# Kernel tuning notes

Hardware: AMD Instinct MI355X
Metric: run time of the kernel (lower is better)

The kernel has to match this reference:

```python
import jax, jax.numpy as jnp
import numpy as np

N = 200_000          # nodes
E = 6_400_000        # directed edges (before self loops)
F_IN, F_OUT = 20, 10
NEG_SLOPE = 0.2      # PyG GATConv default
BN_EPS = 1e-5


def setup_inputs() -> dict:
    key = jax.random.key(0)
    ks = jax.random.split(key, 20)
    s = 0.1
    return {
        "h": jax.random.normal(ks[0], (N, F_IN), jnp.float32),
        "edge_index": jax.random.randint(ks[1], (2, E), 0, N, dtype=jnp.int64),
        "edge_weight": jax.random.uniform(ks[2], (E, 1), dtype=jnp.float32),
        # BatchNorm1d(20) affine params
        "bn_w": jnp.ones((F_IN,), jnp.float32),
        "bn_b": jnp.zeros((F_IN,), jnp.float32),
        # GATConv params (heads=1): lin (no bias), att vectors, edge lin, output bias
        "W": jax.random.normal(ks[3], (F_OUT, F_IN), jnp.float32) * s,
        "att_src": jax.random.normal(ks[4], (F_OUT,), jnp.float32) * s,
        "att_dst": jax.random.normal(ks[5], (F_OUT,), jnp.float32) * s,
        "att_edge": jax.random.normal(ks[6], (F_OUT,), jnp.float32) * s,
        "W_edge": jax.random.normal(ks[7], (F_OUT, 1), jnp.float32) * s,
        "bias": jax.random.normal(ks[8], (F_OUT,), jnp.float32) * s,
        # dense MLP
        "fc1_w": jax.random.normal(ks[9], (F_OUT, F_OUT), jnp.float32) * s,
        "fc1_b": jnp.zeros((F_OUT,), jnp.float32),
        "fc2_w": jax.random.normal(ks[10], (F_OUT, F_OUT), jnp.float32) * s,
        "fc2_b": jnp.zeros((F_OUT,), jnp.float32),
        "fc3_w": jax.random.normal(ks[11], (F_OUT, F_OUT), jnp.float32) * s,
        "fc3_b": jnp.zeros((F_OUT,), jnp.float32),
    }


def reference(h, edge_index, edge_weight, bn_w, bn_b, W, att_src, att_dst,
              att_edge, W_edge, bias, fc1_w, fc1_b, fc2_w, fc2_b, fc3_w, fc3_b):
    # --- BatchNorm1d (training mode: batch stats, biased variance) ---
    mu = h.mean(axis=0)
    var = jnp.var(h, axis=0)
    xn = (h - mu) * jax.lax.rsqrt(var + BN_EPS) * bn_w + bn_b   # [N, 20]

    # --- GATConv (heads=1, edge_dim=1, add_self_loops, fill_value='mean') ---
    xp = xn @ W.T                       # [N, 10] projected node features
    a_s = xp @ att_src                  # [N] per-node source attention term
    a_d = xp @ att_dst                  # [N] per-node dest attention term

    loop = jnp.arange(N, dtype=edge_index.dtype)
    src = jnp.concatenate([edge_index[0], loop])          # [E+N]
    dst = jnp.concatenate([edge_index[1], loop])          # [E+N]
    loop_attr = jnp.broadcast_to(edge_weight.mean(axis=0), (N, 1))
    ea = jnp.concatenate([edge_weight, loop_attr], axis=0)  # [E+N, 1]

    a_e = (ea @ W_edge.T) @ att_edge                       # [E+N]
    logits = jax.nn.leaky_relu(a_s[src] + a_d[dst] + a_e, NEG_SLOPE)

    # segment softmax over destination neighborhoods (every node has a self loop)
    m = jax.ops.segment_max(logits, dst, num_segments=N)
    ex = jnp.exp(logits - m[dst])
    denom = jax.ops.segment_sum(ex, dst, num_segments=N)
    alpha = ex / denom[dst]                                # [E+N]

    msg = xp[src] * alpha[:, None]                         # [E+N, 10]
    out = jax.ops.segment_sum(msg, dst, num_segments=N) + bias  # [N, 10]

    embeddings = jax.nn.relu(out)
    y = jax.nn.relu(out @ fc1_w.T + fc1_b)
    y = jax.nn.relu(y @ fc2_w.T + fc2_b)
    y = y @ fc3_w.T + fc3_b
    return embeddings, y
```

## Files before the change

### kernel.cpp

```cpp
#include <hip/hip_runtime.h>
#include <hip/hip_fp16.h>

#define NN 200000
#define NE 6400000
#define F_IN 20
#define F_OUT 10
#define NEG_SLOPE 0.2f
#define BN_EPS 1e-5f

#define NPB 256
#define NBUCK 782
#define CHUNK 8192
#define NBLK 782
#define SB 512
#define SSB 1024
#define SNPT (CHUNK / SSB)
#define SZ (NBUCK * NBLK)
#define SCANB 1024
#define G1 ((SZ + SCANB - 1) / SCANB)
#define PREB 120
#define RT 1024
#define MAXB 9216
#define CNPT ((MAXB + RT - 1) / RT)

#define OFF_C      41
#define OFF_LOOPAE 42
#define OFF_PART   128
#define OFF_PEW    (OFF_PART + PREB * 40)
#define OFF_AD     (OFF_PEW + NBLK)
#define OFF_XPA    (((OFF_AD + NN) + 3) & ~3)
#define OFF_XPB    (OFF_XPA + 4 * NN)
#define OFF_SCN    (OFF_XPB + 2 * NN)
#define OFF_BS     (OFF_SCN + SZ + 1)
#define OFF_M      (((OFF_BS + 1024) + 1) & ~1)
#define OFF_REC    OFF_M

typedef unsigned long long u64;

__global__ void __launch_bounds__(SB) k_pre(
        const float* __restrict__ h, const int* __restrict__ ei,
        float* __restrict__ part, int* __restrict__ M) {
    int t = threadIdx.x;
    if (blockIdx.x < PREB) {
        float s[F_IN], q[F_IN];
#pragma unroll
        for (int f = 0; f < F_IN; ++f) { s[f] = 0.f; q[f] = 0.f; }
        for (int i = blockIdx.x * SB + t; i < NN; i += PREB * SB) {
            const float4* row = (const float4*)(h + (size_t)i * F_IN);
#pragma unroll
            for (int v = 0; v < 5; ++v) {
                float4 x = row[v];
                int f = v * 4;
                s[f+0] += x.x; q[f+0] += x.x * x.x;
                s[f+1] += x.y; q[f+1] += x.y * x.y;
                s[f+2] += x.z; q[f+2] += x.z * x.z;
                s[f+3] += x.w; q[f+3] += x.w * x.w;
            }
        }
#pragma unroll
        for (int f = 0; f < F_IN; ++f)
            for (int o = 32; o > 0; o >>= 1) {
                s[f] += __shfl_down(s[f], o);
                q[f] += __shfl_down(q[f], o);
            }
        __shared__ float red[8][40];
        int wave = t >> 6, lane = t & 63;
        if (lane == 0) {
#pragma unroll
            for (int f = 0; f < F_IN; ++f) { red[wave][f] = s[f]; red[wave][F_IN + f] = q[f]; }
        }
        __syncthreads();
        if (t < 40) {
            float a = 0.f;
#pragma unroll
            for (int w8 = 0; w8 < 8; ++w8) a += red[w8][t];
            part[blockIdx.x * 40 + t] = a;
        }
    } else {
        __shared__ int hist[NBUCK];
        int blk = blockIdx.x - PREB;
        for (int i = t; i < NBUCK; i += SB) hist[i] = 0;
        __syncthreads();
        int base = blk * CHUNK;
        int lim = NE - base; if (lim > CHUNK) lim = CHUNK;
        for (int j = t; j < lim; j += SB) {
            int dst = ei[NE + base + j];
            atomicAdd(&hist[dst >> 8], 1);
        }
        __syncthreads();
        for (int i = t; i < NBUCK; i += SB) M[i * NBLK + blk] = hist[i];
    }
}

__global__ void k_scan1(const int* __restrict__ M, int* __restrict__ SCN,
                        int* __restrict__ BS) {
    __shared__ int tmp[SCANB];
    int t = threadIdx.x, g = blockIdx.x;
    int idx = g * SCANB + t;
    int v = (idx < SZ) ? M[idx] : 0;
    tmp[t] = v;
    __syncthreads();
    for (int off = 1; off < SCANB; off <<= 1) {
        int x = (t >= off) ? tmp[t - off] : 0;
        __syncthreads();
        tmp[t] += x;
        __syncthreads();
    }
    if (idx < SZ) SCN[idx] = tmp[t] - v;
    if (t == SCANB - 1) BS[g] = tmp[t];
}

__global__ void k_scan2(int* __restrict__ BS) {
    __shared__ int tmp[SCANB];
    int t = threadIdx.x;
    int v = (t < G1) ? BS[t] : 0;
    tmp[t] = v;
    __syncthreads();
    for (int off = 1; off < SCANB; off <<= 1) {
        int x = (t >= off) ? tmp[t - off] : 0;
        __syncthreads();
        tmp[t] += x;
        __syncthreads();
    }
    if (t < G1) BS[t] = tmp[t] - v;
}

__global__ void __launch_bounds__(SSB) k_scatter(
        const int* __restrict__ ei, const float* __restrict__ ew,
        const int* __restrict__ SCN, const int* __restrict__ BS,
        u64* __restrict__ rec, float* __restrict__ pew) {
    __shared__ u64 sBuf[CHUNK];
    __shared__ int sScan[1024];
    __shared__ int sCur[NBUCK];
    __shared__ int sBase[NBUCK];
    __shared__ float redw[16];
    int t = threadIdx.x, blk = blockIdx.x;
    sScan[t] = 0;
    for (int i = t; i < NBUCK; i += SSB) {
        int idx = i * NBLK + blk;
        sBase[i] = SCN[idx] + BS[idx >> 10];
    }
    __syncthreads();
    int base = blk * CHUNK;
    int lim = NE - base; if (lim > CHUNK) lim = CHUNK;
    u64 r[SNPT]; int bk[SNPT];
    float es = 0.f;
#pragma unroll
    for (int k = 0; k < SNPT; ++k) {
        int j = t + k * SSB;
        bk[k] = -1;
        if (j < lim) {
            int e = base + j;
            int src = __builtin_nontemporal_load(ei + e);
            int dst = ei[NE + e];
            float w  = __builtin_nontemporal_load(ew + e);
            es += w;
            int b = dst >> 8;
            bk[k] = b;
            r[k] = ((u64)__float_as_uint(w) << 32) |
                   (u64)(((unsigned)src << 8) | (unsigned)(dst & (NPB - 1)));
            atomicAdd(&sScan[b], 1);
        }
    }
    for (int o = 32; o > 0; o >>= 1) es += __shfl_down(es, o);
    if ((t & 63) == 0) redw[t >> 6] = es;
    __syncthreads();
    if (t == 0) {
        float a = 0.f;
#pragma unroll
        for (int w16 = 0; w16 < 16; ++w16) a += redw[w16];
        pew[blk] = a;
    }
    for (int d = 1; d < 1024; d <<= 1) {
        int idx = (t + 1) * (d << 1) - 1;
        if (idx < 1024) sScan[idx] += sScan[idx - d];
        __syncthreads();
    }
    if (t == 0) sScan[1023] = 0;
    __syncthreads();
    for (int d = 512; d >= 1; d >>= 1) {
        int idx = (t + 1) * (d << 1) - 1;
        if (idx < 1024) {
            int x = sScan[idx - d];
            sScan[idx - d] = sScan[idx];
            sScan[idx] += x;
        }
        __syncthreads();
    }
    for (int i = t; i < NBUCK; i += SSB) sCur[i] = sScan[i];
    __syncthreads();
#pragma unroll
    for (int k = 0; k < SNPT; ++k) {
        if (bk[k] >= 0) {
            int p = atomicAdd(&sCur[bk[k]], 1);
            sBuf[p] = r[k];
        }
    }
    __syncthreads();
    int grp = t >> 3, lane = t & 7;
    for (int b = grp; b < NBUCK; b += SSB / 8) {
        int st = sScan[b];
        int len = sScan[b + 1] - st;
        int gb = sBase[b];
        for (int k2 = lane; k2 < len; k2 += 8)
            rec[gb + k2] = sBuf[st + k2];
    }
}

__global__ void k_node(const float* __restrict__ h, const float* __restrict__ W,
                       const float* __restrict__ att_src, const float* __restrict__ att_dst,
                       const float* __restrict__ bn_w, const float* __restrict__ bn_b,
                       const float* __restrict__ W_edge, const float* __restrict__ att_edge,
                       const float* __restrict__ part, const float* __restrict__ pew,
                       float* __restrict__ ws, __half* __restrict__ xpa,
                       float* __restrict__ xpb, float* __restrict__ a_d) {
    __shared__ float sW[F_OUT * F_IN], sAs[F_OUT], sAd[F_OUT], sSc[F_IN], sSh[F_IN];
    __shared__ float col[40];
    __shared__ float redw[4];
    int t = threadIdx.x;
    if (t < F_OUT * F_IN) sW[t] = W[t];
    if (t < F_OUT) { sAs[t] = att_src[t]; sAd[t] = att_dst[t]; }
    if (t >= 200 && t < 240) {
        int f = t - 200;
        float s = 0.f;
#pragma unroll 8
        for (int b = 0; b < PREB; ++b) s += part[b * 40 + f];
        col[f] = s;
    }
    float es = 0.f;
    for (int i = t; i < NBLK; i += 256) es += pew[i];
    for (int o = 32; o > 0; o >>= 1) es += __shfl_down(es, o);
    if ((t & 63) == 0) redw[t >> 6] = es;
    __syncthreads();
    if (t < F_IN) {
        float mu  = col[t] / (float)NN;
        float var = col[F_IN + t] / (float)NN - mu * mu;
        float sc  = bn_w[t] * rsqrtf(var + BN_EPS);
        sSc[t] = sc;
        sSh[t] = bn_b[t] - mu * sc;
    }
    if (t == 63 && blockIdx.x == 0) {
        float ews = redw[0] + redw[1] + redw[2] + redw[3];
        float c = 0.f;
#pragma unroll
        for (int k = 0; k < F_OUT; ++k) c += W_edge[k] * att_edge[k];
        ws[OFF_C] = c;
        ws[OFF_LOOPAE] = c * (ews / (float)NE);
    }
    __syncthreads();
    int i = blockIdx.x * blockDim.x + t;
    if (i >= NN) return;
    float xn[F_IN];
    const float4* row = (const float4*)(h + (size_t)i * F_IN);
#pragma unroll
    for (int v = 0; v < 5; ++v) {
        float4 x = row[v];
        int f = v * 4;
        xn[f+0] = x.x * sSc[f+0] + sSh[f+0];
        xn[f+1] = x.y * sSc[f+1] + sSh[f+1];
        xn[f+2] = x.z * sSc[f+2] + sSh[f+2];
        xn[f+3] = x.w * sSc[f+3] + sSh[f+3];
    }
    float acc[F_OUT];
    float as = 0.f, ad = 0.f;
#pragma unroll
    for (int k = 0; k < F_OUT; ++k) {
        float a = 0.f;
#pragma unroll
        for (int f = 0; f < F_IN; ++f) a += sW[k * F_IN + f] * xn[f];
        acc[k] = a;
        as += a * sAs[k];
        ad += a * sAd[k];
    }
    __half2 h01 = __floats2half2_rn(acc[0], acc[1]);
    __half2 h23 = __floats2half2_rn(acc[2], acc[3]);
    __half2 h45 = __floats2half2_rn(acc[4], acc[5]);
    __half2 h67 = __floats2half2_rn(acc[6], acc[7]);
    __half2 h89 = __floats2half2_rn(acc[8], acc[9]);
    uint4 U;
    U.x = *(unsigned*)&h01; U.y = *(unsigned*)&h23;
    U.z = *(unsigned*)&h45; U.w = *(unsigned*)&h67;
    *(uint4*)(xpa + (size_t)i * 8) = U;
    uint2 V;
    V.x = *(unsigned*)&h89;
    V.y = __float_as_uint(as);
    *(uint2*)(xpb + (size_t)i * 2) = V;
    a_d[i] = ad;
}

__global__ void __launch_bounds__(RT, 8) k_creduce(
        const float* __restrict__ ws_ro, const int* __restrict__ SCN,
        const int* __restrict__ BS,
        const u64* __restrict__ rec, const __half* __restrict__ xpa,
        const float* __restrict__ xpb, const float* __restrict__ a_d,
        const float* __restrict__ bias,
        const float* __restrict__ fc1w, const float* __restrict__ fc1b,
        const float* __restrict__ fc2w, const float* __restrict__ fc2b,
        const float* __restrict__ fc3w, const float* __restrict__ fc3b,
        float* __restrict__ out) {
    __shared__ u64 sBuf[MAXB];
    __shared__ int sHist[NPB];
    __shared__ int sOff[NPB + 1];
    __shared__ float s1[100], s2[100], s3[100], sb[F_OUT], sb1[F_OUT], sb2[F_OUT], sb3[F_OUT];
    int t = threadIdx.x, b = blockIdx.x;
    if (t < NPB) sHist[t] = 0;
    if (t < 100) { s1[t] = fc1w[t]; s2[t] = fc2w[t]; s3[t] = fc3w[t]; }
    if (t >= 256 && t < 256 + F_OUT) {
        int k = t - 256;
        sb[k] = bias[k]; sb1[k] = fc1b[k]; sb2[k] = fc2b[k]; sb3[k] = fc3b[k];
    }
    __syncthreads();
    int i0 = b * NBLK;
    int start = SCN[i0] + BS[i0 >> 10];
    int end;
    if (b == NBUCK - 1) end = NE;
    else { int i1 = (b + 1) * NBLK; end = SCN[i1] + BS[i1 >> 10]; }
    int cnt = end - start;
    if (cnt > MAXB) cnt = MAXB;
    u64 r[CNPT];
#pragma unroll
    for (int k = 0; k < CNPT; ++k) {
        int i = t + k * RT;
        if (i < cnt) {
            r[k] = __builtin_nontemporal_load(rec + start + i);
            atomicAdd(&sHist[(unsigned)r[k] & (NPB - 1u)], 1);
        }
    }
    __syncthreads();
    int v = (t < NPB) ? sHist[t] : 0;
    for (int off = 1; off < NPB; off <<= 1) {
        int x = (t >= off && t < NPB) ? sHist[t - off] : 0;
        __syncthreads();
        if (t < NPB) sHist[t] += x;
        __syncthreads();
    }
    if (t < NPB) { sOff[t + 1] = sHist[t]; sHist[t] -= v; }
    if (t == 0) sOff[0] = 0;
    __syncthreads();
#pragma unroll
    for (int k = 0; k < CNPT; ++k) {
        int i = t + k * RT;
        if (i < cnt) {
            int p = atomicAdd(&sHist[(unsigned)r[k] & (NPB - 1u)], 1);
            if (p < MAXB) sBuf[p] = r[k];
        }
    }
    __syncthreads();
    int node = t & (NPB - 1);
    int quarter = t >> 8;
    int gnode = b * NPB + node;
    float adn = (gnode < NN) ? a_d[gnode] : 0.f;
    float c = ws_ro[OFF_C];
    const uint4* xpa4 = (const uint4*)xpa;
    const uint2* xpb2 = (const uint2*)xpb;
    int myStart = sOff[node];
    int e0 = sOff[node + 1];
    float den = 0.f;
    float num[F_OUT];
#pragma unroll
    for (int k = 0; k < F_OUT; ++k) num[k] = 0.f;
    int j = myStart + quarter;
    for (; j + 12 < e0; j += 16) {
        u64 r1 = sBuf[j];
        u64 r2 = sBuf[j + 4];
        u64 r3 = sBuf[j + 8];
        u64 r4 = sBuf[j + 12];
        unsigned i1 = (unsigned)r1 >> 8, i2 = (unsigned)r2 >> 8;
        unsigned i3 = (unsigned)r3 >> 8, i4 = (unsigned)r4 >> 8;
        uint4 A1 = xpa4[i1]; uint4 A2 = xpa4[i2];
        uint4 A3 = xpa4[i3]; uint4 A4 = xpa4[i4];
        uint2 B1 = xpb2[i1]; uint2 B2 = xpb2[i2];
        uint2 B3 = xpb2[i3]; uint2 B4 = xpb2[i4];
        float l1 = __uint_as_float(B1.y) + adn + c * __uint_as_float((unsigned)(r1 >> 32));
        float l2 = __uint_as_float(B2.y) + adn + c * __uint_as_float((unsigned)(r2 >> 32));
        float l3 = __uint_as_float(B3.y) + adn + c * __uint_as_float((unsigned)(r3 >> 32));
        float l4 = __uint_as_float(B4.y) + adn + c * __uint_as_float((unsigned)(r4 >> 32));
        l1 = l1 > 0.f ? l1 : NEG_SLOPE * l1;
        l2 = l2 > 0.f ? l2 : NEG_SLOPE * l2;
        l3 = l3 > 0.f ? l3 : NEG_SLOPE * l3;
        l4 = l4 > 0.f ? l4 : NEG_SLOPE * l4;
        float e1 = __expf(l1), e2 = __expf(l2), e3 = __expf(l3), e4 = __expf(l4);
        float2 f0 = __half22float2(*(const __half2*)&A1.x);
        float2 f1 = __half22float2(*(const __half2*)&A1.y);
        float2 f2 = __half22float2(*(const __half2*)&A1.z);
        float2 f3 = __half22float2(*(const __half2*)&A1.w);
        float2 f4 = __half22float2(*(const __half2*)&B1.x);
        float2 g0 = __half22float2(*(const __half2*)&A2.x);
        float2 g1 = __half22float2(*(const __half2*)&A2.y);
        float2 g2 = __half22float2(*(const __half2*)&A2.z);
        float2 g3 = __half22float2(*(const __half2*)&A2.w);
        float2 g4 = __half22float2(*(const __half2*)&B2.x);
        float2 h0 = __half22float2(*(const __half2*)&A3.x);
        float2 h1 = __half22float2(*(const __half2*)&A3.y);
        float2 h2 = __half22float2(*(const __half2*)&A3.z);
        float2 h3 = __half22float2(*(const __half2*)&A3.w);
        float2 h4 = __half22float2(*(const __half2*)&B3.x);
        float2 k0 = __half22float2(*(const __half2*)&A4.x);
        float2 k1 = __half22float2(*(const __half2*)&A4.y);
        float2 k2 = __half22float2(*(const __half2*)&A4.z);
        float2 k3 = __half22float2(*(const __half2*)&A4.w);
        float2 k4 = __half22float2(*(const __half2*)&B4.x);
        den += (e1 + e2) + (e3 + e4);
        num[0] += e1 * f0.x + e2 * g0.x + e3 * h0.x + e4 * k0.x;
        num[1] += e1 * f0.y + e2 * g0.y + e3 * h0.y + e4 * k0.y;
        num[2] += e1 * f1.x + e2 * g1.x + e3 * h1.x + e4 * k1.x;
        num[3] += e1 * f1.y + e2 * g1.y + e3 * h1.y + e4 * k1.y;
        num[4] += e1 * f2.x + e2 * g2.x + e3 * h2.x + e4 * k2.x;
        num[5] += e1 * f2.y + e2 * g2.y + e3 * h2.y + e4 * k2.y;
        num[6] += e1 * f3.x + e2 * g3.x + e3 * h3.x + e4 * k3.x;
        num[7] += e1 * f3.y + e2 * g3.y + e3 * h3.y + e4 * k3.y;
        num[8] += e1 * f4.x + e2 * g4.x + e3 * h4.x + e4 * k4.x;
        num[9] += e1 * f4.y + e2 * g4.y + e3 * h4.y + e4 * k4.y;
    }
    for (; j < e0; j += 4) {
        u64 r1 = sBuf[j];
        unsigned i1 = (unsigned)r1 >> 8;
        uint4 A = xpa4[i1];
        uint2 B = xpb2[i1];
        float l1 = __uint_as_float(B.y) + adn + c * __uint_as_float((unsigned)(r1 >> 32));
        l1 = l1 > 0.f ? l1 : NEG_SLOPE * l1;
        float e1 = __expf(l1);
        float2 f0 = __half22float2(*(const __half2*)&A.x);
        float2 f1 = __half22float2(*(const __half2*)&A.y);
        float2 f2 = __half22float2(*(const __half2*)&A.z);
        float2 f3 = __half22float2(*(const __half2*)&A.w);
        float2 f4 = __half22float2(*(const __half2*)&B.x);
        den += e1;
        num[0] += e1 * f0.x; num[1] += e1 * f0.y;
        num[2] += e1 * f1.x; num[3] += e1 * f1.y;
        num[4] += e1 * f2.x; num[5] += e1 * f2.y;
        num[6] += e1 * f3.x; num[7] += e1 * f3.y;
        num[8] += e1 * f4.x; num[9] += e1 * f4.y;
    }
    __syncthreads();
    float* sP = (float*)sBuf;
    if (quarter) {
        float* p = sP + (node * 3 + (quarter - 1)) * 11;
        p[0] = den;
#pragma unroll
        for (int k = 0; k < F_OUT; ++k) p[1 + k] = num[k];
    }
    __syncthreads();
    if (quarter) return;
#pragma unroll
    for (int q = 0; q < 3; ++q) {
        const float* p = sP + (node * 3 + q) * 11;
        den += p[0];
#pragma unroll
        for (int k = 0; k < F_OUT; ++k) num[k] += p[1 + k];
    }

    if (gnode >= NN) return;
    uint4 An = xpa4[gnode];
    uint2 Bn = xpb2[gnode];
    float l = __uint_as_float(Bn.y) + adn + ws_ro[OFF_LOOPAE];
    l = l > 0.f ? l : NEG_SLOPE * l;
    float exs = __expf(l);
    float inv = 1.0f / (den + exs);
    float xn[F_OUT];
    {
        float2 f0 = __half22float2(*(const __half2*)&An.x);
        float2 f1 = __half22float2(*(const __half2*)&An.y);
        float2 f2 = __half22float2(*(const __half2*)&An.z);
        float2 f3 = __half22float2(*(const __half2*)&An.w);
        float2 f4 = __half22float2(*(const __half2*)&Bn.x);
        xn[0]=f0.x; xn[1]=f0.y; xn[2]=f1.x; xn[3]=f1.y; xn[4]=f2.x;
        xn[5]=f2.y; xn[6]=f3.x; xn[7]=f3.y; xn[8]=f4.x; xn[9]=f4.y;
    }
    float o[F_OUT], y1[F_OUT], y2[F_OUT];
#pragma unroll
    for (int k = 0; k < F_OUT; ++k) {
        o[k] = (num[k] + exs * xn[k]) * inv + sb[k];
        out[(size_t)gnode * F_OUT + k] = fmaxf(o[k], 0.f);
    }
#pragma unroll
    for (int k = 0; k < F_OUT; ++k) {
        float a = sb1[k];
#pragma unroll
        for (int jj = 0; jj < F_OUT; ++jj) a += s1[k * F_OUT + jj] * o[jj];
        y1[k] = fmaxf(a, 0.f);
    }
#pragma unroll
    for (int k = 0; k < F_OUT; ++k) {
        float a = sb2[k];
#pragma unroll
        for (int jj = 0; jj < F_OUT; ++jj) a += s2[k * F_OUT + jj] * y1[jj];
        y2[k] = fmaxf(a, 0.f);
    }
#pragma unroll
    for (int k = 0; k < F_OUT; ++k) {
        float a = sb3[k];
#pragma unroll
        for (int jj = 0; jj < F_OUT; ++jj) a += s3[k * F_OUT + jj] * y2[jj];
        out[(size_t)NN * F_OUT + (size_t)gnode * F_OUT + k] = a;
    }
}

extern "C" void kernel_launch(void* const* d_in, const int* in_sizes, int n_in,
                              void* d_out, int out_size, void* d_ws, size_t ws_size,
                              hipStream_t stream) {
    const float* h        = (const float*)d_in[0];
    const int*   ei       = (const int*)  d_in[1];
    const float* ew       = (const float*)d_in[2];
    const float* bn_w     = (const float*)d_in[3];
    const float* bn_b     = (const float*)d_in[4];
    const float* W        = (const float*)d_in[5];
    const float* att_src  = (const float*)d_in[6];
    const float* att_dst  = (const float*)d_in[7];
    const float* att_edge = (const float*)d_in[8];
    const float* W_edge   = (const float*)d_in[9];
    const float* bias     = (const float*)d_in[10];
    const float* fc1w     = (const float*)d_in[11];
    const float* fc1b     = (const float*)d_in[12];
    const float* fc2w     = (const float*)d_in[13];
    const float* fc2b     = (const float*)d_in[14];
    const float* fc3w     = (const float*)d_in[15];
    const float* fc3b     = (const float*)d_in[16];
    float* ws  = (float*)d_ws;
    int*   wsi = (int*)d_ws;
    float* out = (float*)d_out;
    __half* xpa = (__half*)(ws + OFF_XPA);
    float*  xpb = ws + OFF_XPB;

    k_pre   <<<PREB + NBLK, SB, 0, stream>>>(h, ei, ws + OFF_PART, wsi + OFF_M);
    k_scan1 <<<G1, SCANB, 0, stream>>>(wsi + OFF_M, wsi + OFF_SCN, wsi + OFF_BS);
    k_scan2 <<<1, SCANB, 0, stream>>>(wsi + OFF_BS);
    k_scatter<<<NBLK, SSB, 0, stream>>>(ei, ew, wsi + OFF_SCN, wsi + OFF_BS,
                                        (u64*)(wsi + OFF_REC), ws + OFF_PEW);
    k_node  <<<(NN + 255) / 256, 256, 0, stream>>>(h, W, att_src, att_dst,
                                                   bn_w, bn_b, W_edge, att_edge,
                                                   ws + OFF_PART, ws + OFF_PEW,
                                                   ws, xpa, xpb, ws + OFF_AD);
    k_creduce<<<NBUCK, RT, 0, stream>>>(ws, wsi + OFF_SCN, wsi + OFF_BS,
                                        (const u64*)(wsi + OFF_REC),
                                        xpa, xpb, ws + OFF_AD,
                                        bias, fc1w, fc1b, fc2w, fc2b, fc3w, fc3b, out);
}
```

Before: 319.1 us.

## Use 261-node buckets with 3 threads per node and larger edge chunks

Destination buckets now hold 261 nodes instead of 256, computed with a magic-multiply division. The reduce kernel now uses 3 threads per node instead of 4, so 783 of 1024 threads are active. Edge chunks grow to 8960 with fewer scatter blocks, and the per-bucket global base is read lazily only for non-empty buckets instead of preloaded into shared memory. The goal is fewer blocks and less scan/histogram overhead and fewer partial-sum merges, at the cost of idle threads in the reduce, more serial work per thread, and a larger shared buffer that may lower occupancy.

```diff
diff --git a/kernel.cpp b/kernel.cpp
--- a/kernel.cpp
+++ b/kernel.cpp
@@ -8,20 +8,22 @@
 #define NEG_SLOPE 0.2f
 #define BN_EPS 1e-5f
 
-#define NPB 256
-#define NBUCK 782
-#define CHUNK 8192
-#define NBLK 782
+#define NPB 261
+#define NBUCK 767
+#define ACT (NPB * 3)
+#define CHUNK 8960
+#define NBLK 715
 #define SB 512
 #define SSB 1024
-#define SNPT (CHUNK / SSB)
+#define SNPT 9
 #define SZ (NBUCK * NBLK)
 #define SCANB 1024
 #define G1 ((SZ + SCANB - 1) / SCANB)
 #define PREB 120
 #define RT 1024
-#define MAXB 9216
+#define MAXB 9360
 #define CNPT ((MAXB + RT - 1) / RT)
+#define MAGIC261 16455814ULL
 
 #define OFF_C      41
 #define OFF_LOOPAE 42
@@ -37,6 +39,10 @@
 
 typedef unsigned long long u64;
 
+static __device__ __forceinline__ unsigned div261(unsigned d) {
+    return (unsigned)(((u64)d * MAGIC261) >> 32);
+}
+
 __global__ void __launch_bounds__(SB) k_pre(
         const float* __restrict__ h, const int* __restrict__ ei,
         float* __restrict__ part, int* __restrict__ M) {
@@ -84,8 +90,8 @@
         int base = blk * CHUNK;
         int lim = NE - base; if (lim > CHUNK) lim = CHUNK;
         for (int j = t; j < lim; j += SB) {
-            int dst = ei[NE + base + j];
-            atomicAdd(&hist[dst >> 8], 1);
+            unsigned dst = (unsigned)ei[NE + base + j];
+            atomicAdd(&hist[div261(dst)], 1);
         }
         __syncthreads();
         for (int i = t; i < NBUCK; i += SB) M[i * NBLK + blk] = hist[i];
@@ -132,14 +138,9 @@
     __shared__ u64 sBuf[CHUNK];
     __shared__ int sScan[1024];
     __shared__ int sCur[NBUCK];
-    __shared__ int sBase[NBUCK];
     __shared__ float redw[16];
     int t = threadIdx.x, blk = blockIdx.x;
     sScan[t] = 0;
-    for (int i = t; i < NBUCK; i += SSB) {
-        int idx = i * NBLK + blk;
-        sBase[i] = SCN[idx] + BS[idx >> 10];
-    }
     __syncthreads();
     int base = blk * CHUNK;
     int lim = NE - base; if (lim > CHUNK) lim = CHUNK;
@@ -152,13 +153,14 @@
         if (j < lim) {
             int e = base + j;
             int src = __builtin_nontemporal_load(ei + e);
-            int dst = ei[NE + e];
+            unsigned dst = (unsigned)ei[NE + e];
             float w  = __builtin_nontemporal_load(ew + e);
             es += w;
-            int b = dst >> 8;
-            bk[k] = b;
+            unsigned b = div261(dst);
+            unsigned dlo = dst - b * 261u;
+            bk[k] = (int)b;
             r[k] = ((u64)__float_as_uint(w) << 32) |
-                   (u64)(((unsigned)src << 8) | (unsigned)(dst & (NPB - 1)));
+                   (u64)(((unsigned)src << 9) | dlo);
             atomicAdd(&sScan[b], 1);
         }
     }
@@ -201,7 +203,9 @@
     for (int b = grp; b < NBUCK; b += SSB / 8) {
         int st = sScan[b];
         int len = sScan[b + 1] - st;
-        int gb = sBase[b];
+        if (len == 0) continue;
+        int idx = b * NBLK + blk;
+        int gb = SCN[idx] + BS[idx >> 10];
         for (int k2 = lane; k2 < len; k2 += 8)
             rec[gb + k2] = sBuf[st + k2];
     }
@@ -299,14 +303,14 @@
         const float* __restrict__ fc3w, const float* __restrict__ fc3b,
         float* __restrict__ out) {
     __shared__ u64 sBuf[MAXB];
-    __shared__ int sHist[NPB];
+    __shared__ int sHist[264];
     __shared__ int sOff[NPB + 1];
     __shared__ float s1[100], s2[100], s3[100], sb[F_OUT], sb1[F_OUT], sb2[F_OUT], sb3[F_OUT];
     int t = threadIdx.x, b = blockIdx.x;
     if (t < NPB) sHist[t] = 0;
     if (t < 100) { s1[t] = fc1w[t]; s2[t] = fc2w[t]; s3[t] = fc3w[t]; }
-    if (t >= 256 && t < 256 + F_OUT) {
-        int k = t - 256;
+    if (t >= 512 && t < 512 + F_OUT) {
+        int k = t - 512;
         sb[k] = bias[k]; sb1[k] = fc1b[k]; sb2[k] = fc2b[k]; sb3[k] = fc3b[k];
     }
     __syncthreads();
@@ -323,7 +327,7 @@
         int i = t + k * RT;
         if (i < cnt) {
             r[k] = __builtin_nontemporal_load(rec + start + i);
-            atomicAdd(&sHist[(unsigned)r[k] & (NPB - 1u)], 1);
+            atomicAdd(&sHist[(unsigned)r[k] & 0x1FFu], 1);
         }
     }
     __syncthreads();
@@ -341,32 +345,33 @@
     for (int k = 0; k < CNPT; ++k) {
         int i = t + k * RT;
         if (i < cnt) {
-            int p = atomicAdd(&sHist[(unsigned)r[k] & (NPB - 1u)], 1);
+            int p = atomicAdd(&sHist[(unsigned)r[k] & 0x1FFu], 1);
             if (p < MAXB) sBuf[p] = r[k];
         }
     }
     __syncthreads();
-    int node = t & (NPB - 1);
-    int quarter = t >> 8;
+    int act = (t < ACT);
+    int node = act ? (t / 3) : 0;
+    int third = t - node * 3;
     int gnode = b * NPB + node;
-    float adn = (gnode < NN) ? a_d[gnode] : 0.f;
+    float adn = (act && gnode < NN) ? a_d[gnode] : 0.f;
     float c = ws_ro[OFF_C];
     const uint4* xpa4 = (const uint4*)xpa;
     const uint2* xpb2 = (const uint2*)xpb;
-    int myStart = sOff[node];
-    int e0 = sOff[node + 1];
+    int myStart = act ? sOff[node] : 0;
+    int e0 = act ? sOff[node + 1] : 0;
     float den = 0.f;
     float num[F_OUT];
 #pragma unroll
     for (int k = 0; k < F_OUT; ++k) num[k] = 0.f;
-    int j = myStart + quarter;
-    for (; j + 12 < e0; j += 16) {
+    int j = myStart + third;
+    for (; j + 9 < e0; j += 12) {
         u64 r1 = sBuf[j];
-        u64 r2 = sBuf[j + 4];
-        u64 r3 = sBuf[j + 8];
-        u64 r4 = sBuf[j + 12];
-        unsigned i1 = (unsigned)r1 >> 8, i2 = (unsigned)r2 >> 8;
-        unsigned i3 = (unsigned)r3 >> 8, i4 = (unsigned)r4 >> 8;
+        u64 r2 = sBuf[j + 3];
+        u64 r3 = sBuf[j + 6];
+        u64 r4 = sBuf[j + 9];
+        unsigned i1 = (unsigned)r1 >> 9, i2 = (unsigned)r2 >> 9;
+        unsigned i3 = (unsigned)r3 >> 9, i4 = (unsigned)r4 >> 9;
         uint4 A1 = xpa4[i1]; uint4 A2 = xpa4[i2];
         uint4 A3 = xpa4[i3]; uint4 A4 = xpa4[i4];
         uint2 B1 = xpb2[i1]; uint2 B2 = xpb2[i2];
@@ -412,9 +417,9 @@
         num[8] += e1 * f4.x + e2 * g4.x + e3 * h4.x + e4 * k4.x;
         num[9] += e1 * f4.y + e2 * g4.y + e3 * h4.y + e4 * k4.y;
     }
-    for (; j < e0; j += 4) {
+    for (; j < e0; j += 3) {
         u64 r1 = sBuf[j];
-        unsigned i1 = (unsigned)r1 >> 8;
+        unsigned i1 = (unsigned)r1 >> 9;
         uint4 A = xpa4[i1];
         uint2 B = xpb2[i1];
         float l1 = __uint_as_float(B.y) + adn + c * __uint_as_float((unsigned)(r1 >> 32));
@@ -434,17 +439,17 @@
     }
     __syncthreads();
     float* sP = (float*)sBuf;
-    if (quarter) {
-        float* p = sP + (node * 3 + (quarter - 1)) * 11;
+    if (act && third) {
+        float* p = sP + (node * 2 + (third - 1)) * 11;
         p[0] = den;
 #pragma unroll
         for (int k = 0; k < F_OUT; ++k) p[1 + k] = num[k];
     }
     __syncthreads();
-    if (quarter) return;
-#pragma unroll
-    for (int q = 0; q < 3; ++q) {
-        const float* p = sP + (node * 3 + q) * 11;
+    if (!act || third) return;
+#pragma unroll
+    for (int q = 0; q < 2; ++q) {
+        const float* p = sP + (node * 2 + q) * 11;
         den += p[0];
 #pragma unroll
         for (int k = 0; k < F_OUT; ++k) num[k] += p[1 + k];
```

Result: faster. 311.2 us (-2.5%).
